# Performance work log

Measured on AMD Instinct MI355X. Metric: run time of the kernel, lower is better.

Reference implementation:

```python
import jax, jax.numpy as jnp
import numpy as np

D_MODEL = 128
D_STATE = 256
D_CONV = 4
EXPAND = 2
D_INNER = EXPAND * D_MODEL  # 256 == D_STATE (required by the module's einsum/add)
B = 4
L = 100  # fixed: self.C has first dim 100


def silu(x):
    return x * jax.nn.sigmoid(x)


def setup_inputs() -> dict:
    key = jax.random.key(0)
    ks = jax.random.split(key, 10)
    s = 0.02
    dt_std = D_INNER ** (-0.5)
    inp = {
        "hidden_states": jax.random.normal(ks[0], (B, L, D_MODEL), jnp.float32),
        "state": jax.random.normal(ks[1], (B, L, D_INNER, D_STATE), jnp.float32),
        # torch nn.Linear layout: (out_features, in_features)
        "in_proj_w": jax.random.normal(ks[2], (2 * D_INNER, D_MODEL), jnp.float32) * s,
        "in_proj_b": jnp.zeros((2 * D_INNER,), jnp.float32),
        # depthwise conv1d weight: (d_inner, 1, d_conv)
        "conv_w": jax.random.normal(ks[3], (D_INNER, 1, D_CONV), jnp.float32) * s,
        "conv_b": jnp.zeros((D_INNER,), jnp.float32),
        "x_proj_w": jax.random.normal(ks[4], (2 * D_STATE, D_INNER), jnp.float32) * s,
        "dt_proj_w": jax.random.uniform(ks[5], (D_INNER, D_INNER), jnp.float32, -dt_std, dt_std),
        "dt_proj_b": jnp.zeros((D_INNER,), jnp.float32),
        # A_log = log(arange(1, d_state+1)) broadcast to (d_inner, d_state)
        "A_log": jnp.log(jnp.broadcast_to(jnp.arange(1, D_STATE + 1, dtype=jnp.float32), (D_INNER, D_STATE))),
        "D1": jnp.ones((D_INNER,), jnp.float32),
        # torch inits self.C to ones; add tiny noise to avoid degenerate baseline
        "C_param": jnp.ones((L, D_STATE, D_STATE), jnp.float32) + jax.random.normal(ks[6], (L, D_STATE, D_STATE), jnp.float32) * 0.01,
        "out_proj_w": jax.random.normal(ks[7], (D_MODEL, D_INNER), jnp.float32) * s,
        "out_proj_b": jnp.zeros((D_MODEL,), jnp.float32),
    }
    return inp


def reference(hidden_states, state, in_proj_w, in_proj_b, conv_w, conv_b,
              x_proj_w, dt_proj_w, dt_proj_b, A_log, D1, C_param,
              out_proj_w, out_proj_b):
    b, l, _ = hidden_states.shape
    xz = hidden_states @ in_proj_w.T + in_proj_b          # (b, l, 2*d_inner)
    x, z = jnp.split(xz, 2, axis=-1)                      # each (b, l, d_inner)

    # causal depthwise conv: pad (d_conv-1) left == conv with pad both sides then [:, :, :l]
    xc = jnp.transpose(x, (0, 2, 1))                      # (b, d_inner, l)
    xc = jax.lax.conv_general_dilated(
        xc, conv_w, window_strides=(1,), padding=[(conv_w.shape[-1] - 1, 0)],
        dimension_numbers=("NCH", "OIH", "NCH"), feature_group_count=xc.shape[1])
    xc = xc + conv_b[None, :, None]
    x = silu(jnp.transpose(xc, (0, 2, 1)))                # (b, l, d_inner)

    bc = x @ x_proj_w.T                                   # (b, l, 2*d_state)
    Bm, _Cm_unused = jnp.split(bc, 2, axis=-1)            # torch shadows chunked C with self.C

    dt = jax.nn.softplus(x @ dt_proj_w.T + dt_proj_b)     # (b, l, d_inner)
    A = -jnp.exp(A_log)                                   # (d_inner, d_state)
    dA = jnp.exp(dt[..., None] * A)                       # (b, l, d_inner, d_state)
    dB = dt[..., None] * Bm[..., None, :]                 # (b, l, d_inner, d_state)
    actual_state = state * dA + dB                        # elementwise 'blnd,blnd->blnd'

    y = jnp.einsum("bldn,ldn->bln", actual_state, C_param) + D1 * x  # (b, l, d_inner)
    y = y * silu(z)
    out = y @ out_proj_w.T + out_proj_b                   # (b, l, d_model)
    return out, actual_state
```

## Files before the change

kernel.cpp:

```cpp
#include <hip/hip_runtime.h>

#define LEN 100
#define NR 400

__device__ __forceinline__ float siluf_(float x) { return x / (1.0f + __expf(-x)); }
__device__ __forceinline__ float softplusf_(float x) {
    return (x > 20.f) ? x : log1pf(expf(x));
}

typedef float f4v __attribute__((ext_vector_type(4)));
__device__ __forceinline__ float4 nt_load4(const float* p) {
    f4v t = __builtin_nontemporal_load((const f4v*)p);
    return make_float4(t.x, t.y, t.z, t.w);
}
__device__ __forceinline__ void nt_store4(float* p, float4 v) {
    f4v t; t.x = v.x; t.y = v.y; t.z = v.z; t.w = v.w;
    __builtin_nontemporal_store(t, (f4v*)p);
}

__global__ void __launch_bounds__(256) k_front(
    const float* __restrict__ hidden, const float* __restrict__ ipw, const float* __restrict__ ipb,
    const float* __restrict__ cw, const float* __restrict__ cb,
    const float* __restrict__ xpw, const float* __restrict__ dtw, const float* __restrict__ dtb,
    float* __restrict__ xact, float* __restrict__ Bm, float* __restrict__ dt,
    float* __restrict__ zs)
{
    int r = blockIdx.x;
    int l = r % LEN;
    int j = threadIdx.x;
    int lb = l < 3 ? l : 3;
    __shared__ float hid[4][128];
    __shared__ __align__(16) float xs[256];

    for (int e = j; e < 512; e += 256) {
        int k = e >> 7;
        int c = e & 127;
        hid[k][c] = (k <= lb) ? hidden[(size_t)(r - k) * 128 + c] : 0.f;
    }
    __syncthreads();

    float b0 = ipb[j];
    float xp0 = b0, xp1 = b0, xp2 = b0, xp3 = b0;
    float z = ipb[256 + j];
    const float* wx = ipw + (size_t)j * 128;
    const float* wz = ipw + (size_t)(256 + j) * 128;
#pragma unroll 8
    for (int c = 0; c < 128; c += 4) {
        float4 w = *(const float4*)(wx + c);
        xp0 += w.x * hid[0][c] + w.y * hid[0][c+1] + w.z * hid[0][c+2] + w.w * hid[0][c+3];
        xp1 += w.x * hid[1][c] + w.y * hid[1][c+1] + w.z * hid[1][c+2] + w.w * hid[1][c+3];
        xp2 += w.x * hid[2][c] + w.y * hid[2][c+1] + w.z * hid[2][c+2] + w.w * hid[2][c+3];
        xp3 += w.x * hid[3][c] + w.y * hid[3][c+1] + w.z * hid[3][c+2] + w.w * hid[3][c+3];
        float4 v = *(const float4*)(wz + c);
        z += v.x * hid[0][c] + v.y * hid[0][c+1] + v.z * hid[0][c+2] + v.w * hid[0][c+3];
    }
    float4 w4 = *(const float4*)(cw + j * 4);
    float conv = cb[j] + w4.w * xp0;
    if (lb >= 1) conv += w4.z * xp1;
    if (lb >= 2) conv += w4.y * xp2;
    if (lb >= 3) conv += w4.x * xp3;
    float xa = siluf_(conv);
    xs[j] = xa;
    xact[r * 256 + j] = xa;
    zs[r * 256 + j] = siluf_(z);
    __syncthreads();

    float accB = 0.f, accD = dtb[j];
    const float* bw = xpw + (size_t)j * 256;
    const float* dw = dtw + (size_t)j * 256;
#pragma unroll 8
    for (int c = 0; c < 256; c += 4) {
        float4 bwv = *(const float4*)(bw + c);
        float4 dwv = *(const float4*)(dw + c);
        float4 xv  = *(const float4*)(xs + c);
        accB += bwv.x * xv.x + bwv.y * xv.y + bwv.z * xv.z + bwv.w * xv.w;
        accD += dwv.x * xv.x + dwv.y * xv.y + dwv.z * xv.z + dwv.w * xv.w;
    }
    Bm[r * 256 + j] = accB;
    dt[r * 256 + j] = softplusf_(accD);
}

__global__ void __launch_bounds__(256, 4) k_scan(
    const float* __restrict__ state, const float* __restrict__ alog,
    const float* __restrict__ Cp, const float* __restrict__ dtg,
    const float* __restrict__ Bm, float* __restrict__ ostate, float* __restrict__ ypart)
{
    int bid = blockIdx.x;
    int l = bid >> 4, sl = bid & 15;
    int tid = threadIdx.x;
    int wid = tid >> 6, lane = tid & 63, n0 = lane * 4;
    int d0 = sl * 16 + wid * 4;

    const float* cp = Cp + ((size_t)(l * 256 + d0)) * 256 + n0;
    const float* ap = alog + (size_t)d0 * 256 + n0;

    float4 Bv[4], dtq[4], acc[4];
    size_t soff[4];
#pragma unroll
    for (int b = 0; b < 4; ++b) {
        int r = b * LEN + l;
        Bv[b] = *(const float4*)(Bm + r * 256 + n0);
        dtq[b] = *(const float4*)(dtg + r * 256 + d0);
        soff[b] = ((size_t)(r * 256 + d0)) * 256 + n0;
        acc[b] = make_float4(0.f, 0.f, 0.f, 0.f);
    }

#pragma unroll
    for (int i = 0; i < 4; ++i) {
        float4 av = *(const float4*)(ap + (size_t)i * 256);
        float4 cv = *(const float4*)(cp + (size_t)i * 256);
        float4 na;
        na.x = -expf(av.x); na.y = -expf(av.y);
        na.z = -expf(av.z); na.w = -expf(av.w);
#pragma unroll
        for (int b = 0; b < 4; ++b) {
            float dtv = (i == 0) ? dtq[b].x : (i == 1) ? dtq[b].y
                      : (i == 2) ? dtq[b].z : dtq[b].w;
            float4 s = nt_load4(state + soff[b] + (size_t)i * 256);
            float4 as;
            as.x = s.x * __expf(dtv * na.x) + dtv * Bv[b].x;
            as.y = s.y * __expf(dtv * na.y) + dtv * Bv[b].y;
            as.z = s.z * __expf(dtv * na.z) + dtv * Bv[b].z;
            as.w = s.w * __expf(dtv * na.w) + dtv * Bv[b].w;
            nt_store4(ostate + soff[b] + (size_t)i * 256, as);
            acc[b].x += as.x * cv.x;
            acc[b].y += as.y * cv.y;
            acc[b].z += as.z * cv.z;
            acc[b].w += as.w * cv.w;
        }
    }

    __shared__ __align__(16) float accs[4][4][256];
#pragma unroll
    for (int b = 0; b < 4; ++b)
        *(float4*)(&accs[wid][b][n0]) = acc[b];
    __syncthreads();
    {
        float4 t0 = *(const float4*)(&accs[0][wid][n0]);
        float4 t1 = *(const float4*)(&accs[1][wid][n0]);
        float4 t2 = *(const float4*)(&accs[2][wid][n0]);
        float4 t3 = *(const float4*)(&accs[3][wid][n0]);
        float4 o;
        o.x = (t0.x + t1.x) + (t2.x + t3.x);
        o.y = (t0.y + t1.y) + (t2.y + t3.y);
        o.z = (t0.z + t1.z) + (t2.z + t3.z);
        o.w = (t0.w + t1.w) + (t2.w + t3.w);
        *(float4*)(ypart + ((size_t)(sl * NR + wid * LEN + l)) * 256 + n0) = o;
    }
}

__global__ void __launch_bounds__(256) k_back(
    const float* __restrict__ ypart, const float* __restrict__ xact,
    const float* __restrict__ zs, const float* __restrict__ D1,
    const float* __restrict__ ow, const float* __restrict__ ob,
    float* __restrict__ out)
{
    int r = blockIdx.x;
    int t = threadIdx.x;
    __shared__ __align__(16) float ys[256];
    const int S = NR * 256;
    int idx = r * 256 + t;
    float v = 0.f;
#pragma unroll
    for (int q = 0; q < 16; q++) v += ypart[q * S + idx];
    v += D1[t] * xact[idx];
    v *= zs[idx];
    ys[t] = v;
    __syncthreads();
    if (t < 128) {
        const float* wp = ow + (size_t)t * 256;
        float acc = ob[t];
#pragma unroll 8
        for (int c = 0; c < 256; c += 4) {
            float4 w = *(const float4*)(wp + c);
            float4 x = *(const float4*)(ys + c);
            acc += w.x * x.x + w.y * x.y + w.z * x.z + w.w * x.w;
        }
        out[r * 128 + t] = acc;
    }
}

extern "C" void kernel_launch(void* const* d_in, const int* in_sizes, int n_in,
                              void* d_out, int out_size, void* d_ws, size_t ws_size,
                              hipStream_t stream) {
    const float* hidden = (const float*)d_in[0];
    const float* state  = (const float*)d_in[1];
    const float* ipw    = (const float*)d_in[2];
    const float* ipb    = (const float*)d_in[3];
    const float* cw     = (const float*)d_in[4];
    const float* cb     = (const float*)d_in[5];
    const float* xpw    = (const float*)d_in[6];
    const float* dtw    = (const float*)d_in[7];
    const float* dtb    = (const float*)d_in[8];
    const float* alog   = (const float*)d_in[9];
    const float* D1     = (const float*)d_in[10];
    const float* Cp     = (const float*)d_in[11];
    const float* opw    = (const float*)d_in[12];
    const float* opb    = (const float*)d_in[13];

    float* out    = (float*)d_out;
    float* ostate = out + 51200;

    float* ws    = (float*)d_ws;
    float* xact  = ws;
    float* Bm    = ws + 102400;
    float* dt    = ws + 204800;
    float* zs    = ws + 307200;
    float* ypart = ws + 409600;

    k_front<<<400,  256, 0, stream>>>(hidden, ipw, ipb, cw, cb, xpw, dtw, dtb,
                                      xact, Bm, dt, zs);
    k_scan <<<1600, 256, 0, stream>>>(state, alog, Cp, dt, Bm, ostate, ypart);
    k_back <<<400,  256, 0, stream>>>(ypart, xact, zs, D1, opw, opb, out);
}
```

Before: 281.9 us.

## Batch four sequences per block in front/back kernels to reuse weights

The front and back kernels now give each block one sequence position and process all four batch rows, so every projection weight load is reused four times instead of reloaded per row. The back kernel splits the output projection across both thread halves and reduces the halves through shared memory. The scan kernel also loads C with nontemporal hints and uses the fast exp for A. The price is 4x fewer blocks in the small kernels (100 blocks on a GPU with many CUs) and more registers per thread.

```diff
diff --git a/kernel.cpp b/kernel.cpp
--- a/kernel.cpp
+++ b/kernel.cpp
@@ -25,59 +25,89 @@
     float* __restrict__ xact, float* __restrict__ Bm, float* __restrict__ dt,
     float* __restrict__ zs)
 {
-    int r = blockIdx.x;
-    int l = r % LEN;
+    int l = blockIdx.x;
     int j = threadIdx.x;
     int lb = l < 3 ? l : 3;
-    __shared__ float hid[4][128];
-    __shared__ __align__(16) float xs[256];
-
-    for (int e = j; e < 512; e += 256) {
-        int k = e >> 7;
+    __shared__ __align__(16) float hid[4][4][128];
+    __shared__ __align__(16) float xs[4][256];
+
+    for (int e = j; e < 2048; e += 256) {
+        int b = e >> 9;
+        int k = (e >> 7) & 3;
         int c = e & 127;
-        hid[k][c] = (k <= lb) ? hidden[(size_t)(r - k) * 128 + c] : 0.f;
+        int r = b * LEN + l;
+        hid[b][k][c] = (k <= lb) ? hidden[(size_t)(r - k) * 128 + c] : 0.f;
     }
     __syncthreads();
 
     float b0 = ipb[j];
-    float xp0 = b0, xp1 = b0, xp2 = b0, xp3 = b0;
-    float z = ipb[256 + j];
+    float bz = ipb[256 + j];
+    float xp[4][4];
+    float zz[4];
+#pragma unroll
+    for (int b = 0; b < 4; ++b) {
+        xp[b][0] = b0; xp[b][1] = b0; xp[b][2] = b0; xp[b][3] = b0;
+        zz[b] = bz;
+    }
     const float* wx = ipw + (size_t)j * 128;
     const float* wz = ipw + (size_t)(256 + j) * 128;
-#pragma unroll 8
+#pragma unroll 4
     for (int c = 0; c < 128; c += 4) {
         float4 w = *(const float4*)(wx + c);
-        xp0 += w.x * hid[0][c] + w.y * hid[0][c+1] + w.z * hid[0][c+2] + w.w * hid[0][c+3];
-        xp1 += w.x * hid[1][c] + w.y * hid[1][c+1] + w.z * hid[1][c+2] + w.w * hid[1][c+3];
-        xp2 += w.x * hid[2][c] + w.y * hid[2][c+1] + w.z * hid[2][c+2] + w.w * hid[2][c+3];
-        xp3 += w.x * hid[3][c] + w.y * hid[3][c+1] + w.z * hid[3][c+2] + w.w * hid[3][c+3];
         float4 v = *(const float4*)(wz + c);
-        z += v.x * hid[0][c] + v.y * hid[0][c+1] + v.z * hid[0][c+2] + v.w * hid[0][c+3];
-    }
+#pragma unroll
+        for (int b = 0; b < 4; ++b) {
+            float4 h0 = *(const float4*)(&hid[b][0][c]);
+            float4 h1 = *(const float4*)(&hid[b][1][c]);
+            float4 h2 = *(const float4*)(&hid[b][2][c]);
+            float4 h3 = *(const float4*)(&hid[b][3][c]);
+            xp[b][0] += w.x * h0.x + w.y * h0.y + w.z * h0.z + w.w * h0.w;
+            xp[b][1] += w.x * h1.x + w.y * h1.y + w.z * h1.z + w.w * h1.w;
+            xp[b][2] += w.x * h2.x + w.y * h2.y + w.z * h2.z + w.w * h2.w;
+            xp[b][3] += w.x * h3.x + w.y * h3.y + w.z * h3.z + w.w * h3.w;
+            zz[b]    += v.x * h0.x + v.y * h0.y + v.z * h0.z + v.w * h0.w;
+        }
+    }
+
     float4 w4 = *(const float4*)(cw + j * 4);
-    float conv = cb[j] + w4.w * xp0;
-    if (lb >= 1) conv += w4.z * xp1;
-    if (lb >= 2) conv += w4.y * xp2;
-    if (lb >= 3) conv += w4.x * xp3;
-    float xa = siluf_(conv);
-    xs[j] = xa;
-    xact[r * 256 + j] = xa;
-    zs[r * 256 + j] = siluf_(z);
-    __syncthreads();
-
-    float accB = 0.f, accD = dtb[j];
+    float cbj = cb[j];
+#pragma unroll
+    for (int b = 0; b < 4; ++b) {
+        float conv = cbj + w4.w * xp[b][0];
+        if (lb >= 1) conv += w4.z * xp[b][1];
+        if (lb >= 2) conv += w4.y * xp[b][2];
+        if (lb >= 3) conv += w4.x * xp[b][3];
+        float xa = siluf_(conv);
+        xs[b][j] = xa;
+        int r = b * LEN + l;
+        xact[r * 256 + j] = xa;
+        zs[r * 256 + j] = siluf_(zz[b]);
+    }
+    __syncthreads();
+
+    float accB[4], accD[4];
+    float dtbj = dtb[j];
+#pragma unroll
+    for (int b = 0; b < 4; ++b) { accB[b] = 0.f; accD[b] = dtbj; }
     const float* bw = xpw + (size_t)j * 256;
     const float* dw = dtw + (size_t)j * 256;
 #pragma unroll 8
     for (int c = 0; c < 256; c += 4) {
         float4 bwv = *(const float4*)(bw + c);
         float4 dwv = *(const float4*)(dw + c);
-        float4 xv  = *(const float4*)(xs + c);
-        accB += bwv.x * xv.x + bwv.y * xv.y + bwv.z * xv.z + bwv.w * xv.w;
-        accD += dwv.x * xv.x + dwv.y * xv.y + dwv.z * xv.z + dwv.w * xv.w;
-    }
-    Bm[r * 256 + j] = accB;
-    dt[r * 256 + j] = softplusf_(accD);
+#pragma unroll
+        for (int b = 0; b < 4; ++b) {
+            float4 xv = *(const float4*)(&xs[b][c]);
+            accB[b] += bwv.x * xv.x + bwv.y * xv.y + bwv.z * xv.z + bwv.w * xv.w;
+            accD[b] += dwv.x * xv.x + dwv.y * xv.y + dwv.z * xv.z + dwv.w * xv.w;
+        }
+    }
+#pragma unroll
+    for (int b = 0; b < 4; ++b) {
+        int r = b * LEN + l;
+        Bm[r * 256 + j] = accB[b];
+        dt[r * 256 + j] = softplusf_(accD[b]);
+    }
 }
 
 __global__ void __launch_bounds__(256, 4) k_scan(
@@ -108,10 +138,10 @@
 #pragma unroll
     for (int i = 0; i < 4; ++i) {
         float4 av = *(const float4*)(ap + (size_t)i * 256);
-        float4 cv = *(const float4*)(cp + (size_t)i * 256);
+        float4 cv = nt_load4(cp + (size_t)i * 256);
         float4 na;
-        na.x = -expf(av.x); na.y = -expf(av.y);
-        na.z = -expf(av.z); na.w = -expf(av.w);
+        na.x = -__expf(av.x); na.y = -__expf(av.y);
+        na.z = -__expf(av.z); na.w = -__expf(av.w);
 #pragma unroll
         for (int b = 0; b < 4; ++b) {
             float dtv = (i == 0) ? dtq[b].x : (i == 1) ? dtq[b].y
@@ -155,28 +185,48 @@
     const float* __restrict__ ow, const float* __restrict__ ob,
     float* __restrict__ out)
 {
-    int r = blockIdx.x;
+    int l = blockIdx.x;
     int t = threadIdx.x;
-    __shared__ __align__(16) float ys[256];
+    __shared__ __align__(16) float ys[4][256];
+    __shared__ float ph[4][256];
     const int S = NR * 256;
-    int idx = r * 256 + t;
-    float v = 0.f;
-#pragma unroll
-    for (int q = 0; q < 16; q++) v += ypart[q * S + idx];
-    v += D1[t] * xact[idx];
-    v *= zs[idx];
-    ys[t] = v;
+    float d1 = D1[t];
+#pragma unroll
+    for (int b = 0; b < 4; ++b) {
+        int idx = (b * LEN + l) * 256 + t;
+        float v = 0.f;
+#pragma unroll
+        for (int q = 0; q < 16; q++) v += ypart[q * S + idx];
+        v += d1 * xact[idx];
+        v *= zs[idx];
+        ys[b][t] = v;
+    }
+    __syncthreads();
+    {
+        int j = t & 127;
+        int h = t >> 7;
+        const float* wp = ow + (size_t)j * 256 + h * 128;
+        float bias = (h == 0) ? ob[j] : 0.f;
+        float acc[4];
+#pragma unroll
+        for (int b = 0; b < 4; ++b) acc[b] = bias;
+#pragma unroll 8
+        for (int c = 0; c < 128; c += 4) {
+            float4 w = *(const float4*)(wp + c);
+#pragma unroll
+            for (int b = 0; b < 4; ++b) {
+                float4 x = *(const float4*)(&ys[b][h * 128 + c]);
+                acc[b] += w.x * x.x + w.y * x.y + w.z * x.z + w.w * x.w;
+            }
+        }
+#pragma unroll
+        for (int b = 0; b < 4; ++b) ph[b][t] = acc[b];
+    }
     __syncthreads();
     if (t < 128) {
-        const float* wp = ow + (size_t)t * 256;
-        float acc = ob[t];
-#pragma unroll 8
-        for (int c = 0; c < 256; c += 4) {
-            float4 w = *(const float4*)(wp + c);
-            float4 x = *(const float4*)(ys + c);
-            acc += w.x * x.x + w.y * x.y + w.z * x.z + w.w * x.w;
-        }
-        out[r * 128 + t] = acc;
+#pragma unroll
+        for (int b = 0; b < 4; ++b)
+            out[((size_t)(b * LEN + l)) * 128 + t] = ph[b][t] + ph[b][t + 128];
     }
 }
 
@@ -208,8 +258,8 @@
     float* zs    = ws + 307200;
     float* ypart = ws + 409600;
 
-    k_front<<<400,  256, 0, stream>>>(hidden, ipw, ipb, cw, cb, xpw, dtw, dtb,
-                                      xact, Bm, dt, zs);
+    k_front<<<100, 256, 0, stream>>>(hidden, ipw, ipb, cw, cb, xpw, dtw, dtb,
+                                     xact, Bm, dt, zs);
     k_scan <<<1600, 256, 0, stream>>>(state, alog, Cp, dt, Bm, ostate, ypart);
-    k_back <<<400,  256, 0, stream>>>(ypart, xact, zs, D1, opw, opb, out);
-}
+    k_back <<<100, 256, 0, stream>>>(ypart, xact, zs, D1, opw, opb, out);
+}
```

New measurement: 281.1 us. About the same (-0.3%).
